# Kernel tuning notes

Measured on AMD Instinct MI355X. Metric: run time of the kernel, lower is better.

## Reference

```python
import jax, jax.numpy as jnp
import numpy as np

NX, NU, NY = 128, 64, 32
N = 262144          # batch of state/input samples
GAMMA = 1.0
EPS = 1e-4          # self.eps in the torch module


def _psd_sqrtm(M):
    # differentiable matrix square root for a symmetric PSD matrix
    w, V = jnp.linalg.eigh(M)
    return (V * jnp.sqrt(jnp.clip(w, 0.0))) @ V.T


def setup_inputs() -> dict:
    key = jax.random.key(0)
    ks = jax.random.split(key, 7)
    u = jax.random.normal(ks[0], (N, NU), jnp.float32)
    x = jax.random.normal(ks[1], (N, NX), jnp.float32)
    # geotorch positive_definite(Q), positive_definite(P): materialize PSD matrices
    Mq = jax.random.normal(ks[2], (NX, NX), jnp.float32) / np.float32(np.sqrt(NX))
    Q = Mq @ Mq.T + 1e-2 * jnp.eye(NX, dtype=jnp.float32)
    Mp = jax.random.normal(ks[3], (NX, NX), jnp.float32) / np.float32(np.sqrt(NX))
    P = Mp @ Mp.T + 1e-2 * jnp.eye(NX, dtype=jnp.float32)
    # geotorch skew(S)
    Ms = jax.random.normal(ks[4], (NX, NX), jnp.float32)
    S = 0.5 * (Ms - Ms.T)
    G = jax.random.normal(ks[5], (NY, NX), jnp.float32)
    H = jax.random.normal(ks[6], (NX, NU), jnp.float32)
    return {"u": u, "x": x, "Q": Q, "P": P, "S": S, "G": G, "H": H}


def reference(u, x, Q, P, S, G, H):
    # Htilde = H / (1.01 * sqrt(||H H^T||_2)), spectral norm
    denom = 1.01 * jnp.sqrt(jnp.linalg.norm(H @ H.T, ord=2))
    Htilde = H / denom
    I = jnp.eye(NX, dtype=Q.dtype)
    Asym = -0.5 * (Q + G.T @ G + EPS * I)
    A = (Asym + S) @ P                      # (nx, nx)
    B = GAMMA * (_psd_sqrtm(Q) @ Htilde)    # (nx, nu)
    C = G @ P                               # (ny, nx)
    dx = x @ A.T + u @ B.T                  # (N, nx)
    y = x @ C.T                             # (N, ny)
    return dx, y
```

## Files before the change

### kernel.cpp

```cpp
#include <hip/hip_runtime.h>
#include <hip/hip_bf16.h>


#define NB 262144

typedef __attribute__((ext_vector_type(8))) short s8v;
typedef __attribute__((ext_vector_type(4))) short s4v;
typedef __attribute__((ext_vector_type(4))) float f4v;

__device__ __forceinline__ float bf2f(unsigned short s) {
  unsigned int u = ((unsigned int)s) << 16;
  return __uint_as_float(u);
}
__device__ __forceinline__ unsigned short f2bf(float f) {
  unsigned int u = __float_as_uint(f);
  u += 0x7fffu + ((u >> 16) & 1u);
  return (unsigned short)(u >> 16);
}

__global__ __launch_bounds__(256) void k_prep1(
    const float* __restrict__ Q, const float* __restrict__ S,
    const float* __restrict__ G, const float* __restrict__ H,
    float* __restrict__ Mf, float* __restrict__ HtH, unsigned short* __restrict__ W)
{
  const int bid = blockIdx.x, tid = threadIdx.x;
  if (bid < 64) {
    const int idx = bid * 256 + tid;
    const int j = idx >> 7, k = idx & 127;
    float g = 0.f;
    #pragma unroll 4
    for (int i = 0; i < 32; ++i)
      g += G[i * 128 + j] * G[i * 128 + k];
    Mf[idx] = -0.5f * (Q[idx] + g + ((j == k) ? 1e-4f : 0.f)) + S[idx];
  } else {
    const int e = (bid - 64) * 256 + tid;
    const int a = e >> 6, b = e & 63;
    float s = 0.f;
    #pragma unroll 4
    for (int r = 0; r < 128; ++r)
      s += H[r * 64 + a] * H[r * 64 + b];
    HtH[e] = s;
    if (bid == 64) {
      for (int i = 0; i < 8; ++i) {
        int e2 = i * 256 + tid;
        int n = 128 + (e2 >> 6), kk = 128 + (e2 & 63);
        W[n * 192 + kk] = 0;
      }
    }
  }
}

__global__ __launch_bounds__(256) void k_prepAC(
    const float* __restrict__ Mf, const float* __restrict__ P,
    const float* __restrict__ G, unsigned short* __restrict__ W)
{
  const int bid = blockIdx.x, tid = threadIdx.x;
  if (bid < 64) {
    const int idx = bid * 256 + tid;
    const int n = idx >> 7, k = idx & 127;
    float s = 0.f;
    #pragma unroll 4
    for (int l = 0; l < 128; ++l)
      s += Mf[n * 128 + l] * P[l * 128 + k];
    W[n * 192 + k] = f2bf(s);
  } else {
    for (int i = 0; i < 4; ++i) {
      int e = (bid - 64) * 1024 + i * 256 + tid;
      int j = e >> 7, k = e & 127;
      float s = 0.f;
      #pragma unroll 4
      for (int l = 0; l < 128; ++l)
        s += G[j * 128 + l] * P[l * 128 + k];
      W[(128 + j) * 192 + k] = f2bf(s);
    }
  }
}

__global__ __launch_bounds__(1024) void k_prep23(
    const float* __restrict__ Qg, const float* __restrict__ Hg,
    const float* __restrict__ HtHg, unsigned short* __restrict__ W)
{
  __shared__ char smem[65536];
  unsigned short* Xs = (unsigned short*)smem;
  unsigned short* V0s = (unsigned short*)(smem + 32768);
  unsigned short* V1s = (unsigned short*)(smem + 49152);
  float* vQ = (float*)(smem + 32768);
  float* wQ = (float*)(smem + 33280);
  float* vH = (float*)(smem + 33792);
  float* wH = (float*)(smem + 34048);
  float* red = (float*)(smem + 34304);
  float* HtHs = (float*)(smem + 49152);

  const int tid = threadIdx.x;
  const int lane = tid & 63;
  const int wv = tid >> 6;

  for (int i = 0; i < 16; ++i) {
    int e = i * 1024 + tid;
    int m = e >> 7, k = e & 127;
    Xs[m * 128 + (((k >> 3) ^ (m & 7)) << 3) + (k & 7)] = f2bf(Qg[e]);
  }
  for (int i = 0; i < 4; ++i) HtHs[i * 1024 + tid] = HtHg[i * 1024 + tid];
  if (tid < 128) vQ[tid] = (float)((tid * 1103515245u + 12345u) & 0xffffu) * (1.f / 65536.f) + 0.05f;
  if (tid < 64)  vH[tid] = (float)((tid * 2654435761u + 911u) & 0xffffu) * (1.f / 65536.f) + 0.05f;
  __syncthreads();

  float lamQ = 1.f;
  {
    const int row = tid >> 3, sub = tid & 7;
    for (int it = 0; it < 24; ++it) {
      const s8v q0 = *(const s8v*)&Xs[row * 128 + ((((sub * 2)    ) ^ (row & 7)) << 3)];
      const s8v q1 = *(const s8v*)&Xs[row * 128 + ((((sub * 2) + 1) ^ (row & 7)) << 3)];
      float p = 0.f;
      #pragma unroll
      for (int j = 0; j < 8; ++j) p += bf2f((unsigned short)q0[j]) * vQ[sub * 16 + j];
      #pragma unroll
      for (int j = 0; j < 8; ++j) p += bf2f((unsigned short)q1[j]) * vQ[sub * 16 + 8 + j];
      p += __shfl_xor(p, 1); p += __shfl_xor(p, 2); p += __shfl_xor(p, 4);
      if (sub == 0) wQ[row] = p;
      __syncthreads();
      if (tid < 64) {
        float s = wQ[tid] * wQ[tid] + wQ[tid + 64] * wQ[tid + 64];
        s += __shfl_xor(s, 1); s += __shfl_xor(s, 2); s += __shfl_xor(s, 4);
        s += __shfl_xor(s, 8); s += __shfl_xor(s, 16); s += __shfl_xor(s, 32);
        if (tid == 0) red[0] = sqrtf(s);
      }
      __syncthreads();
      lamQ = red[0];
      if (tid < 128) vQ[tid] = wQ[tid] / lamQ;
      __syncthreads();
    }
  }
  const float bb = 1.10f * lamQ;
  const float sqrtb = sqrtf(bb);

  float lamH = 1.f;
  {
    const int row = tid >> 4, sub = tid & 15;
    for (int it = 0; it < 24; ++it) {
      const f4v h = *(const f4v*)&HtHs[row * 64 + sub * 4];
      float p = h[0] * vH[sub * 4] + h[1] * vH[sub * 4 + 1] + h[2] * vH[sub * 4 + 2] + h[3] * vH[sub * 4 + 3];
      p += __shfl_xor(p, 1); p += __shfl_xor(p, 2); p += __shfl_xor(p, 4); p += __shfl_xor(p, 8);
      if (sub == 0) wH[row] = p;
      __syncthreads();
      if (tid < 64) {
        float s = wH[tid] * wH[tid];
        s += __shfl_xor(s, 1); s += __shfl_xor(s, 2); s += __shfl_xor(s, 4);
        s += __shfl_xor(s, 8); s += __shfl_xor(s, 16); s += __shfl_xor(s, 32);
        if (tid == 0) red[0] = sqrtf(s);
      }
      __syncthreads();
      lamH = red[0];
      if (tid < 64) vH[tid] = wH[tid] / lamH;
      __syncthreads();
    }
  }
  const float invden = 1.f / (1.01f * sqrtf(lamH));
  __syncthreads();

  for (int i = 0; i < 16; ++i) {
    int e = i * 1024 + tid;
    int m = e >> 7, k = e & 127;
    int a = m * 128 + (((k >> 3) ^ (m & 7)) << 3) + (k & 7);
    float q = bf2f(Xs[a]);
    Xs[a] = f2bf(q * (2.f / bb) - ((m == k) ? 1.f : 0.f));
  }
  for (int i = 0; i < 8; ++i) {
    int e = i * 1024 + tid;
    int j = e & 63, m = e >> 6;
    V0s[j * 128 + (((m >> 3) ^ (j & 7)) << 3) + (m & 7)] = f2bf(Hg[m * 64 + j] * invden);
  }
  const int t0 = wv * 2;
  float baccR[2][4];
  #pragma unroll
  for (int tt = 0; tt < 2; ++tt) {
    int mt = (t0 + tt) >> 2, nt = (t0 + tt) & 3;
    int n = nt * 16 + (lane & 15);
    int mb = mt * 16 + ((lane >> 4) << 2);
    #pragma unroll
    for (int i = 0; i < 4; ++i)
      baccR[tt][i] = 0.63661977f * Hg[(mb + i) * 64 + n] * invden;
  }
  __syncthreads();

  unsigned short* Vc = V0s;
  unsigned short* Vp = V1s;
  for (int k = 1; k <= 32; ++k) {
    const float ck = ((k & 1) ? 1.0f : -1.0f) / (3.14159265f * ((float)(k * k) - 0.25f));
    #pragma unroll
    for (int tt = 0; tt < 2; ++tt) {
      const int mt = (t0 + tt) >> 2, nt = (t0 + tt) & 3;
      f4v acc = {0.f, 0.f, 0.f, 0.f};
      const int arow = mt * 16 + (lane & 15);
      const int brow = nt * 16 + (lane & 15);
      #pragma unroll
      for (int ks = 0; ks < 4; ++ks) {
        int kc = ks * 4 + (lane >> 4);
        s8v af = *(const s8v*)&Xs[arow * 128 + ((kc ^ (arow & 7)) << 3)];
        s8v bf = *(const s8v*)&Vc[brow * 128 + ((kc ^ (brow & 7)) << 3)];
        acc = __builtin_amdgcn_mfma_f32_16x16x32_bf16(af, bf, acc, 0, 0, 0);
      }
      const int n = brow;
      const int mb = mt * 16 + ((lane >> 4) << 2);
      const int vaddr = n * 128 + (((mb >> 3) ^ (n & 7)) << 3) + (mb & 7);
      float nv[4];
      if (k == 1) {
        #pragma unroll
        for (int i = 0; i < 4; ++i) nv[i] = acc[i];
      } else {
        s4v ov = *(const s4v*)&Vp[vaddr];
        #pragma unroll
        for (int i = 0; i < 4; ++i) nv[i] = 2.f * acc[i] - bf2f((unsigned short)ov[i]);
      }
      s4v st;
      #pragma unroll
      for (int i = 0; i < 4; ++i) { st[i] = (short)f2bf(nv[i]); baccR[tt][i] += ck * nv[i]; }
      *(s4v*)&Vp[vaddr] = st;
    }
    __syncthreads();
    unsigned short* t = Vc; Vc = Vp; Vp = t;
  }

  #pragma unroll
  for (int tt = 0; tt < 2; ++tt) {
    const int mt = (t0 + tt) >> 2, nt = (t0 + tt) & 3;
    const int n = nt * 16 + (lane & 15);
    const int mb = mt * 16 + ((lane >> 4) << 2);
    #pragma unroll
    for (int i = 0; i < 4; ++i)
      W[(mb + i) * 192 + 128 + n] = f2bf(sqrtb * baccR[tt][i]);
  }
}

__global__ __launch_bounds__(256, 2) void k_main(
    const float* __restrict__ x, const float* __restrict__ u,
    const unsigned short* __restrict__ W, float* __restrict__ out)
{
  __shared__ char smraw[128 * 200 * 2];
  unsigned short* sm = (unsigned short*)smraw;
  float* fb = (float*)smraw;

  const int tid = threadIdx.x, lane = tid & 63, w = tid >> 6;
  const int mw = w & 1, nw = w >> 1;
  const int base = blockIdx.x * 128;

  s8v wf[5][6];
  {
    const int n0 = nw * 80 + (lane & 15);
    const int kof = (lane >> 4) * 8;
    #pragma unroll
    for (int nt = 0; nt < 5; ++nt)
      #pragma unroll
      for (int ks = 0; ks < 6; ++ks)
        wf[nt][ks] = *(const s8v*)&W[(n0 + nt * 16) * 192 + ks * 32 + kof];
  }
  #pragma unroll
  for (int p = 0; p < 16; ++p) {
    int g = p * 256 + tid; int r = g >> 5, c = g & 31;
    f4v v = *(const f4v*)&x[(size_t)(base + r) * 128 + c * 4];
    s4v b;
    #pragma unroll
    for (int i = 0; i < 4; ++i) b[i] = (short)f2bf(v[i]);
    *(s4v*)&sm[r * 200 + c * 4] = b;
  }
  #pragma unroll
  for (int p = 0; p < 8; ++p) {
    int g = p * 256 + tid; int r = g >> 4, c = g & 15;
    f4v v = *(const f4v*)&u[(size_t)(base + r) * 64 + c * 4];
    s4v b;
    #pragma unroll
    for (int i = 0; i < 4; ++i) b[i] = (short)f2bf(v[i]);
    *(s4v*)&sm[r * 200 + 128 + c * 4] = b;
  }
  __syncthreads();

  f4v acc[4][5];
  #pragma unroll
  for (int mt = 0; mt < 4; ++mt)
    #pragma unroll
    for (int nt = 0; nt < 5; ++nt)
      acc[mt][nt] = (f4v){0.f, 0.f, 0.f, 0.f};

  #pragma unroll
  for (int mt = 0; mt < 4; ++mt) {
    const int row = mw * 64 + mt * 16 + (lane & 15);
    const int kof = (lane >> 4) * 8;
    #pragma unroll
    for (int ks = 0; ks < 6; ++ks) {
      s8v af = *(const s8v*)&sm[row * 200 + ks * 32 + kof];
      #pragma unroll
      for (int nt = 0; nt < 5; ++nt)
        acc[mt][nt] = __builtin_amdgcn_mfma_f32_16x16x32_bf16(af, wf[nt][ks], acc[mt][nt], 0, 0, 0);
    }
  }

  float* const yout = out + (size_t)NB * 128;
  #pragma unroll
  for (int pass = 0; pass < 2; ++pass) {
    __syncthreads();
    if (mw == pass) {
      #pragma unroll
      for (int mt = 0; mt < 4; ++mt)
        #pragma unroll
        for (int nt = 0; nt < 5; ++nt) {
          const int rr = mt * 16 + ((lane >> 4) << 2);
          const int cc = nw * 80 + nt * 16 + (lane & 15);
          #pragma unroll
          for (int i = 0; i < 4; ++i)
            fb[(rr + i) * 164 + cc] = acc[mt][nt][i];
        }
    }
    __syncthreads();
    const int rb = base + pass * 64;
    #pragma unroll
    for (int p = 0; p < 8; ++p) {
      int g = p * 256 + tid; int r = g >> 5, c = g & 31;
      *(f4v*)&out[(size_t)(rb + r) * 128 + c * 4] = *(const f4v*)&fb[r * 164 + c * 4];
    }
    #pragma unroll
    for (int p = 0; p < 2; ++p) {
      int g = p * 256 + tid; int r = g >> 3, c = g & 7;
      *(f4v*)&yout[(size_t)(rb + r) * 32 + c * 4] = *(const f4v*)&fb[r * 164 + 128 + c * 4];
    }
  }
}

extern "C" void kernel_launch(void* const* d_in, const int* in_sizes, int n_in,
                              void* d_out, int out_size, void* d_ws, size_t ws_size,
                              hipStream_t stream) {
  const float *u = nullptr, *x = nullptr, *G = nullptr, *H = nullptr;
  const float* sq[3] = {nullptr, nullptr, nullptr};
  int nsq = 0;
  for (int i = 0; i < n_in; ++i) {
    const float* p = (const float*)d_in[i];
    switch (in_sizes[i]) {
      case NB * 64:  u = p; break;
      case NB * 128: x = p; break;
      case 32 * 128: G = p; break;
      case 128 * 64: H = p; break;
      case 128 * 128: if (nsq < 3) sq[nsq++] = p; break;
      default: break;
    }
  }
  const float* Q = sq[0];
  const float* P = sq[1];
  const float* S = sq[2];

  char* ws = (char*)d_ws;
  unsigned short* W = (unsigned short*)ws;
  float* HtH = (float*)(ws + 61440);
  float* Mf  = (float*)(ws + 77824);
  float* out = (float*)d_out;

  k_prep1 <<<80,   256,  0, stream>>>(Q, S, G, H, Mf, HtH, W);
  k_prepAC<<<68,   256,  0, stream>>>(Mf, P, G, W);
  k_prep23<<<1,    1024, 0, stream>>>(Q, H, HtH, W);
  k_main  <<<2048, 256,  0, stream>>>(x, u, W, out);
}
```

Baseline: 433.6 us.

## Fuse Q and H power iterations, drop per-iteration normalization, raise main occupancy

Runs the two power iterations (spectral norms of Q and H^T H) together in one loop, split across thread groups, with a single barrier per iteration. The per-iteration norm reduction and division are replaced by one fixed mid-loop rescale plus a pre-scale of H^T H, and the eigenvalue is recovered as the ratio of the last two iterate norms. This removes most of the barriers on the serial prep path. The trade-off is that overflow safety now depends on the fixed scale factors matching the expected input magnitudes, and the iteration count rises to 32. The main kernel's launch bound also moves to three blocks per SM, which may force fewer registers and cause spills.

After: 492.1 us. 13.5% more time.

```diff
diff --git a/kernel.cpp b/kernel.cpp
--- a/kernel.cpp
+++ b/kernel.cpp
@@ -100,62 +100,75 @@
     int m = e >> 7, k = e & 127;
     Xs[m * 128 + (((k >> 3) ^ (m & 7)) << 3) + (k & 7)] = f2bf(Qg[e]);
   }
-  for (int i = 0; i < 4; ++i) HtHs[i * 1024 + tid] = HtHg[i * 1024 + tid];
+  for (int i = 0; i < 4; ++i) HtHs[i * 1024 + tid] = HtHg[i * 1024 + tid] * 0.00390625f;
   if (tid < 128) vQ[tid] = (float)((tid * 1103515245u + 12345u) & 0xffffu) * (1.f / 65536.f) + 0.05f;
   if (tid < 64)  vH[tid] = (float)((tid * 2654435761u + 911u) & 0xffffu) * (1.f / 65536.f) + 0.05f;
   __syncthreads();
 
-  float lamQ = 1.f;
+  float* qin = vQ; float* qout = wQ;
+  float* hin = vH; float* hout = wH;
+  for (int it = 0; it < 32; ++it) {
+    if (tid < 512) {
+      const int row = tid >> 2, sub = tid & 3;
+      float p = 0.f;
+      #pragma unroll
+      for (int c = 0; c < 4; ++c) {
+        const int ch = sub * 4 + c;
+        const s8v q = *(const s8v*)&Xs[row * 128 + ((ch ^ (row & 7)) << 3)];
+        const f4v a = *(const f4v*)&qin[ch * 8];
+        const f4v b = *(const f4v*)&qin[ch * 8 + 4];
+        p += bf2f((unsigned short)q[0]) * a[0];
+        p += bf2f((unsigned short)q[1]) * a[1];
+        p += bf2f((unsigned short)q[2]) * a[2];
+        p += bf2f((unsigned short)q[3]) * a[3];
+        p += bf2f((unsigned short)q[4]) * b[0];
+        p += bf2f((unsigned short)q[5]) * b[1];
+        p += bf2f((unsigned short)q[6]) * b[2];
+        p += bf2f((unsigned short)q[7]) * b[3];
+      }
+      p += __shfl_xor(p, 1); p += __shfl_xor(p, 2);
+      if (it == 16) p *= 0x1p-32f;
+      if (sub == 0) qout[row] = p;
+    } else {
+      const int idx = tid - 512;
+      const int row = idx >> 3, sub = idx & 7;
+      const f4v a  = *(const f4v*)&HtHs[row * 64 + sub * 8];
+      const f4v b  = *(const f4v*)&HtHs[row * 64 + sub * 8 + 4];
+      const f4v va = *(const f4v*)&hin[sub * 8];
+      const f4v vb = *(const f4v*)&hin[sub * 8 + 4];
+      float p = a[0] * va[0] + a[1] * va[1] + a[2] * va[2] + a[3] * va[3]
+              + b[0] * vb[0] + b[1] * vb[1] + b[2] * vb[2] + b[3] * vb[3];
+      p += __shfl_xor(p, 1); p += __shfl_xor(p, 2); p += __shfl_xor(p, 4);
+      if (it == 16) p *= 0x1p-8f;
+      if (sub == 0) hout[row] = p;
+    }
+    __syncthreads();
+    float* t;
+    t = qin; qin = qout; qout = t;
+    t = hin; hin = hout; hout = t;
+  }
+
   {
-    const int row = tid >> 3, sub = tid & 7;
-    for (int it = 0; it < 24; ++it) {
-      const s8v q0 = *(const s8v*)&Xs[row * 128 + ((((sub * 2)    ) ^ (row & 7)) << 3)];
-      const s8v q1 = *(const s8v*)&Xs[row * 128 + ((((sub * 2) + 1) ^ (row & 7)) << 3)];
-      float p = 0.f;
-      #pragma unroll
-      for (int j = 0; j < 8; ++j) p += bf2f((unsigned short)q0[j]) * vQ[sub * 16 + j];
-      #pragma unroll
-      for (int j = 0; j < 8; ++j) p += bf2f((unsigned short)q1[j]) * vQ[sub * 16 + 8 + j];
-      p += __shfl_xor(p, 1); p += __shfl_xor(p, 2); p += __shfl_xor(p, 4);
-      if (sub == 0) wQ[row] = p;
-      __syncthreads();
-      if (tid < 64) {
-        float s = wQ[tid] * wQ[tid] + wQ[tid + 64] * wQ[tid + 64];
-        s += __shfl_xor(s, 1); s += __shfl_xor(s, 2); s += __shfl_xor(s, 4);
-        s += __shfl_xor(s, 8); s += __shfl_xor(s, 16); s += __shfl_xor(s, 32);
-        if (tid == 0) red[0] = sqrtf(s);
-      }
-      __syncthreads();
-      lamQ = red[0];
-      if (tid < 128) vQ[tid] = wQ[tid] / lamQ;
-      __syncthreads();
-    }
-  }
-  const float bb = 1.10f * lamQ;
+    float s = 0.f;
+    if (wv == 0)      { float a = qin[lane],  b = qin[lane + 64];  s = a * a + b * b; }
+    else if (wv == 1) { float a = qout[lane], b = qout[lane + 64]; s = a * a + b * b; }
+    else if (wv == 2) { float a = hin[lane];  s = a * a; }
+    else if (wv == 3) { float a = hout[lane]; s = a * a; }
+    if (wv < 4) {
+      s += __shfl_xor(s, 1); s += __shfl_xor(s, 2); s += __shfl_xor(s, 4);
+      s += __shfl_xor(s, 8); s += __shfl_xor(s, 16); s += __shfl_xor(s, 32);
+      if (lane == 0) red[wv] = s;
+    }
+  }
+  __syncthreads();
+  if (tid == 0) {
+    red[4] = sqrtf(red[0] / red[1]);
+    red[5] = 256.f * sqrtf(red[2] / red[3]);
+  }
+  __syncthreads();
+  const float bb = 1.10f * red[4];
   const float sqrtb = sqrtf(bb);
-
-  float lamH = 1.f;
-  {
-    const int row = tid >> 4, sub = tid & 15;
-    for (int it = 0; it < 24; ++it) {
-      const f4v h = *(const f4v*)&HtHs[row * 64 + sub * 4];
-      float p = h[0] * vH[sub * 4] + h[1] * vH[sub * 4 + 1] + h[2] * vH[sub * 4 + 2] + h[3] * vH[sub * 4 + 3];
-      p += __shfl_xor(p, 1); p += __shfl_xor(p, 2); p += __shfl_xor(p, 4); p += __shfl_xor(p, 8);
-      if (sub == 0) wH[row] = p;
-      __syncthreads();
-      if (tid < 64) {
-        float s = wH[tid] * wH[tid];
-        s += __shfl_xor(s, 1); s += __shfl_xor(s, 2); s += __shfl_xor(s, 4);
-        s += __shfl_xor(s, 8); s += __shfl_xor(s, 16); s += __shfl_xor(s, 32);
-        if (tid == 0) red[0] = sqrtf(s);
-      }
-      __syncthreads();
-      lamH = red[0];
-      if (tid < 64) vH[tid] = wH[tid] / lamH;
-      __syncthreads();
-    }
-  }
-  const float invden = 1.f / (1.01f * sqrtf(lamH));
+  const float invden = 1.f / (1.01f * sqrtf(red[5]));
   __syncthreads();
 
   for (int i = 0; i < 16; ++i) {
@@ -232,7 +245,7 @@
   }
 }
 
-__global__ __launch_bounds__(256, 2) void k_main(
+__global__ __launch_bounds__(256, 3) void k_main(
     const float* __restrict__ x, const float* __restrict__ u,
     const unsigned short* __restrict__ W, float* __restrict__ out)
 {
```
